# Kernel tuning notes

Hardware: AMD Instinct MI355X
Metric: run time of the kernel (lower is better)

## Reference

```python
import jax, jax.numpy as jnp
import numpy as np

HEADS = 4
DIM_HEAD = 32


def _ln(x, g, b):
    m = x.mean(-1, keepdims=True)
    v = ((x - m) ** 2).mean(-1, keepdims=True)
    return (x - m) * jax.lax.rsqrt(v + 1e-5) * g + b


def setup_inputs() -> dict:
    key = jax.random.key(0)
    ks = jax.random.split(key, 9)
    b, n, X, Y, W1, W2, d = 4, 6, 10, 10, 10, 10, 128
    x, y, w1, w2 = 10, 10, 4, 4
    inner = HEADS * DIM_HEAD  # 128 == d
    init = 0.02
    return {
        "q": jax.random.normal(ks[0], (b, n, X, Y, W1, W2, d), jnp.float32),
        "k": jax.random.normal(ks[1], (b, n, x, y, w1, w2, d), jnp.float32),
        "v": jax.random.normal(ks[2], (b, n, x, y, w1, w2, d), jnp.float32),
        "skip": jax.random.normal(ks[3], (b, X, Y, W1, W2, d), jnp.float32),
        "head_gate": jax.random.uniform(ks[4], (HEADS,), jnp.float32, 0.5, 1.5),
        "ln_q_g": jnp.ones((d,), jnp.float32), "ln_q_b": jnp.zeros((d,), jnp.float32),
        "ln_k_g": jnp.ones((d,), jnp.float32), "ln_k_b": jnp.zeros((d,), jnp.float32),
        "ln_v_g": jnp.ones((d,), jnp.float32), "ln_v_b": jnp.zeros((d,), jnp.float32),
        "wq": jax.random.normal(ks[5], (d, inner), jnp.float32) * init,
        "bq": jnp.zeros((inner,), jnp.float32),
        "wk": jax.random.normal(ks[6], (d, inner), jnp.float32) * init,
        "bk": jnp.zeros((inner,), jnp.float32),
        "wv": jax.random.normal(ks[7], (d, inner), jnp.float32) * init,
        "bv": jnp.zeros((inner,), jnp.float32),
        "wp": jax.random.normal(ks[8], (inner, d), jnp.float32) * init,
        "bp": jnp.zeros((d,), jnp.float32),
    }


def reference(q, k, v, skip, head_gate,
              ln_q_g, ln_q_b, ln_k_g, ln_k_b, ln_v_g, ln_v_b,
              wq, bq, wk, bk, wv, bv, wp, bp):
    b, n, X, Y, W1, W2, d = q.shape
    _, _, x, y, w1, w2, _ = k.shape
    L = X * Y                      # number of windows (== x*y, asserted in torch)
    Qn = n * W1 * W2               # query tokens per window (views folded in)
    Kn = n * w1 * w2               # kv tokens per window
    # 'b n x y w1 w2 d -> b (x y) (n w1 w2) d'
    qf = q.transpose(0, 2, 3, 1, 4, 5, 6).reshape(b, L, Qn, d)
    kf = k.transpose(0, 2, 3, 1, 4, 5, 6).reshape(b, L, Kn, d)
    vf = v.transpose(0, 2, 3, 1, 4, 5, 6).reshape(b, L, Kn, d)
    # pre-norm + linear qkv projections
    qh = (_ln(qf, ln_q_g, ln_q_b) @ wq + bq).reshape(b, L, Qn, HEADS, DIM_HEAD)
    kh = (_ln(kf, ln_k_g, ln_k_b) @ wk + bk).reshape(b, L, Kn, HEADS, DIM_HEAD)
    vh = (_ln(vf, ln_v_g, ln_v_b) @ wv + bv).reshape(b, L, Kn, HEADS, DIM_HEAD)
    scale = DIM_HEAD ** -0.5
    # windowed attention scores: (b, m, L, Q, K)
    dot = jnp.einsum('blqmd,blkmd->bmlqk', qh * scale, kh)
    dot = dot * head_gate[None, :, None, None, None]  # multiplicative head gate pre-softmax
    att = jax.nn.softmax(dot, axis=-1)
    a = jnp.einsum('bmlqk,blkmd->blqmd', att, vh).reshape(b, L, Qn, HEADS * DIM_HEAD)
    # 'b (x y) (n w1 w2) c -> b n x y w1 w2 c'
    out = a.reshape(b, X, Y, n, W1, W2, HEADS * DIM_HEAD).transpose(0, 3, 1, 2, 4, 5, 6)
    z = out @ wp + bp
    z = z.mean(axis=1)             # mean-pool over views
    return z + skip
```

## Files before the change

kernel.cpp:

```cpp
#include <hip/hip_runtime.h>
#include <hip/hip_bf16.h>

#define DEV __device__ __forceinline__

typedef __attribute__((ext_vector_type(8))) short short8;
typedef __attribute__((ext_vector_type(8))) unsigned short ushort8;
typedef __attribute__((ext_vector_type(4))) float f32x4;
typedef __attribute__((ext_vector_type(2))) unsigned int uint2v;

DEV unsigned short f2bf(float f) {
    unsigned u = __float_as_uint(f);
    unsigned r = u + 0x7fffu + ((u >> 16) & 1u);
    return (unsigned short)(r >> 16);
}
DEV unsigned cvt_pk_bf16(float lo, float hi) {
    unsigned r;
    asm("v_cvt_pk_bf16_f32 %0, %1, %2" : "=v"(r) : "v"(lo), "v"(hi));
    return r;
}
#define GLDS16(gp, lp)                                                              \
    __builtin_amdgcn_global_load_lds(                                               \
        (const __attribute__((address_space(1))) void*)(gp),                        \
        (__attribute__((address_space(3))) void*)(lp), 16, 0, 0)


__global__ __launch_bounds__(128) void prep_kernel(
    const float* __restrict__ wq, const float* __restrict__ wk,
    const float* __restrict__ wv, const float* __restrict__ wp,
    const float* __restrict__ ln_q_g, const float* __restrict__ ln_q_b,
    const float* __restrict__ ln_k_g, const float* __restrict__ ln_k_b,
    const float* __restrict__ ln_v_g, const float* __restrict__ ln_v_b,
    const float* __restrict__ bq, const float* __restrict__ bk,
    const float* __restrict__ bv, const float* __restrict__ bp,
    const float* __restrict__ head_gate,
    unsigned short* __restrict__ Wt, float* __restrict__ b2)
{
    const int set = blockIdx.x / 9, sub = blockIdx.x % 9;
    const float* W    = set == 0 ? wq : set == 1 ? wk : set == 2 ? wv : wp;
    const float* g    = set == 0 ? ln_q_g : set == 1 ? ln_k_g : ln_v_g;
    const float* e    = set == 0 ? ln_q_b : set == 1 ? ln_k_b : ln_v_b;
    const float* bias = set == 0 ? bq : set == 1 ? bk : set == 2 ? bv : bp;
    const int mode = set == 0 ? 2 : (set == 3 ? 0 : 1);
    const float scale = 0.17677669529663687f;

    if (sub == 0) {
        const int col = threadIdx.x;
        float sg = (mode == 2) ? scale * head_gate[col >> 5] : 1.f;
        float esum = 0.f;
        if (mode >= 1) {
#pragma unroll 8
            for (int k = 0; k < 128; ++k) esum += e[k] * W[k * 128 + col];
        }
        b2[set * 128 + col] = (bias[col] + esum) * sg;
    } else {
        const int k = threadIdx.x;
        const float gk = (mode >= 1) ? g[k] : 1.f;
        const int kk = k >> 5, h = (k >> 3) & 3, j = k & 7;
#pragma unroll
        for (int c = 0; c < 16; ++c) {
            int col = (sub - 1) * 16 + c;
            int nt = col >> 4, q15 = col & 15;
            float sg = (mode == 2) ? scale * head_gate[col >> 5] : 1.f;
            long idx = set * 16384 + (((nt * 4 + kk) * 64 + q15 * 4 + h) << 3) + j;
            Wt[idx] = f2bf(W[k * 128 + col] * gk * sg);
        }
    }
}

__global__ __launch_bounds__(256) void qkv_proj_mfma(
    const float* __restrict__ qsrc, const float* __restrict__ ksrc, const float* __restrict__ vsrc,
    const unsigned short* __restrict__ WtAll, const float* __restrict__ b2All,
    unsigned short* __restrict__ qh, unsigned short* __restrict__ kh, unsigned short* __restrict__ vh)
{
    __shared__ unsigned short WtL[16384];

    const int bid = blockIdx.x;
    const int tid = threadIdx.x;
    const int w = tid >> 6, lane = tid & 63;
    const int q15 = lane & 15, h = lane >> 4;

    const float* src; unsigned short* dst; int set, isQ, grp;
    if (bid < 4200)      { src = qsrc; dst = qh; set = 0; isQ = 1; grp = bid * 4 + w; }
    else if (bid < 4800) { src = ksrc; dst = kh; set = 1; isQ = 0; grp = (bid - 4200) * 4 + w; }
    else                 { src = vsrc; dst = vh; set = 2; isQ = 0; grp = (bid - 4800) * 4 + w; }
    const unsigned short* WtF = WtAll + set * 16384;
    const float* b2 = b2All + set * 128;

#pragma unroll
    for (int i = 0; i < 8; ++i)
        GLDS16(WtF + i * 2048 + tid * 8, &WtL[i * 2048 + w * 512]);

    int so;
    if (isQ) {
        int bl = grp / 42, rem = grp % 42;
        int nn = rem / 7, t = rem % 7;
        int rc = t * 16 + q15; if (rc > 99) rc = 99;
        int b = bl / 100, l = bl % 100;
        int Xi = l / 10, Yi = l % 10;
        int wA = rc / 10, wB = rc % 10;
        so = ((((b * 6 + nn) * 10 + Xi) * 10 + Yi) * 10 + wA) * 10 + wB;
    } else {
        int bl = grp / 6, nn = grp % 6;
        int b = bl / 100, l = bl % 100;
        int Xi = l / 10, Yi = l % 10;
        int wA = q15 >> 2, wB = q15 & 3;
        so = ((((b * 6 + nn) * 10 + Xi) * 10 + Yi) * 4 + wA) * 4 + wB;
    }

    float x[4][8];
    {
        const float* row = src + (long)so * 128 + h * 8;
#pragma unroll
        for (int kk = 0; kk < 4; ++kk) {
            f32x4 a = *(const f32x4*)(row + kk * 32);
            f32x4 b = *(const f32x4*)(row + kk * 32 + 4);
            x[kk][0] = a[0]; x[kk][1] = a[1]; x[kk][2] = a[2]; x[kk][3] = a[3];
            x[kk][4] = b[0]; x[kk][5] = b[1]; x[kk][6] = b[2]; x[kk][7] = b[3];
        }
    }

    float s = 0.f, s2 = 0.f;
#pragma unroll
    for (int kk = 0; kk < 4; ++kk)
#pragma unroll
        for (int j = 0; j < 8; ++j) { s += x[kk][j]; s2 += x[kk][j] * x[kk][j]; }
    s  += __shfl_xor(s, 16);  s  += __shfl_xor(s, 32);
    s2 += __shfl_xor(s2, 16); s2 += __shfl_xor(s2, 32);
    const float mean = s * (1.f / 128.f);
    const float var  = s2 * (1.f / 128.f) - mean * mean;
    const float rs  = rsqrtf(var + 1e-5f);
    const float mrs = -mean * rs;

    short8 xf[4];
#pragma unroll
    for (int kk = 0; kk < 4; ++kk) {
        union { unsigned u[4]; short8 s8; } cv;
#pragma unroll
        for (int d = 0; d < 4; ++d)
            cv.u[d] = cvt_pk_bf16(fmaf(x[kk][2 * d], rs, mrs), fmaf(x[kk][2 * d + 1], rs, mrs));
        xf[kk] = cv.s8;
    }

    f32x4 acc[8];
#pragma unroll
    for (int nt = 0; nt < 8; ++nt)
        acc[nt] = *(const f32x4*)(b2 + nt * 16 + h * 4);

    __syncthreads();

#pragma unroll
    for (int kk = 0; kk < 4; ++kk)
#pragma unroll
        for (int nt = 0; nt < 8; ++nt) {
            short8 wf = *(const short8*)&WtL[(((nt * 4 + kk) * 64) + lane) * 8];
            acc[nt] = __builtin_amdgcn_mfma_f32_16x16x32_bf16(wf, xf[kk], acc[nt], 0, 0, 0);
        }

    unsigned short* og = dst + (long)grp * 1024;
#pragma unroll
    for (int nt = 0; nt < 8; ++nt) {
        uint2v pk;
        pk.x = cvt_pk_bf16(acc[nt][0], acc[nt][1]);
        pk.y = cvt_pk_bf16(acc[nt][2], acc[nt][3]);
        *(uint2v*)(og + (nt * 64 + q15 * 4 + h) * 4) = pk;
    }
}

__global__ __launch_bounds__(256, 3) void attn_mfma_kernel(
    const unsigned short* __restrict__ qh, const unsigned short* __restrict__ kh,
    const unsigned short* __restrict__ vh, unsigned short* __restrict__ am)
{
    __shared__ unsigned short Vt[32 * 104];
    __shared__ unsigned short Pt[4][2][16 * 104];

    const int tid = threadIdx.x;
    const int half = blockIdx.x & 1;
    const int m  = (blockIdx.x >> 1) & 3;
    const int bl = blockIdx.x >> 3;
    const int w = tid >> 6, lane = tid & 63;
    const int q15 = lane & 15, h = lane >> 4;
    const int t = half * 4 + w;

    const int coff = (((2 * m + (h >> 1)) * 64) + q15 * 4 + 2 * (h & 1)) * 4;

    short8 kf[6];
#pragma unroll
    for (int ntk = 0; ntk < 6; ++ntk)
        kf[ntk] = *(const short8*)(kh + (long)(bl * 6 + ntk) * 1024 + coff);

    {
        const int d = tid & 31, kt0 = tid >> 5;
        const int f = m * 32 + d;
        const int ntv = f >> 4, hp = (f >> 2) & 3, rg = f & 3;
#pragma unroll
        for (int j = 0; j < 12; ++j) {
            int kt = kt0 + 8 * j;
            Vt[d * 104 + kt] =
                vh[(long)(bl * 6 + (kt >> 4)) * 1024 + ((ntv * 64 + (kt & 15) * 4 + hp) << 2) + rg];
        }
    }
    __syncthreads();

    short8 vf[2][3];
#pragma unroll
    for (int dt = 0; dt < 2; ++dt)
#pragma unroll
        for (int ks = 0; ks < 3; ++ks)
            vf[dt][ks] = *(const short8*)(Vt + (dt * 16 + q15) * 104 + ks * 32 + h * 8);

    if (t >= 7) return;

    const long qgBase = (long)(bl * 6) * 7 * 1024;

    f32x4 o0 = {0.f, 0.f, 0.f, 0.f}, o1 = {0.f, 0.f, 0.f, 0.f};

#pragma unroll
    for (int nn = 0; nn < 6; ++nn) {
        unsigned short* ptw = &Pt[w][nn & 1][0];

        short8 qf = *(const short8*)(qh + qgBase + (long)(nn * 7 + t) * 1024 + coff);

        f32x4 sc[6];
#pragma unroll
        for (int nt = 0; nt < 6; ++nt)
            sc[nt] = __builtin_amdgcn_mfma_f32_16x16x32_bf16(kf[nt], qf, (f32x4){0.f, 0.f, 0.f, 0.f}, 0, 0, 0);

        float p[24];
#pragma unroll
        for (int nt = 0; nt < 6; ++nt)
#pragma unroll
            for (int rg = 0; rg < 4; ++rg)
                p[nt * 4 + rg] = __expf(sc[nt][rg]);

#pragma unroll
        for (int nt = 0; nt < 6; ++nt) {
            uint2v pk;
            pk.x = cvt_pk_bf16(p[nt * 4 + 0], p[nt * 4 + 1]);
            pk.y = cvt_pk_bf16(p[nt * 4 + 2], p[nt * 4 + 3]);
            *(uint2v*)(ptw + q15 * 104 + nt * 16 + h * 4) = pk;
        }

        float s01 = (p[0] + p[1]) + (p[2] + p[3]);
        float s23 = (p[4] + p[5]) + (p[6] + p[7]);
        float s45 = (p[8] + p[9]) + (p[10] + p[11]);
        float s67 = (p[12] + p[13]) + (p[14] + p[15]);
        float s89 = (p[16] + p[17]) + (p[18] + p[19]);
        float sab = (p[20] + p[21]) + (p[22] + p[23]);
        float sum = ((s01 + s23) + (s45 + s67)) + (s89 + sab);
        sum += __shfl_xor(sum, 16);
        sum += __shfl_xor(sum, 32);
        const float inv = __builtin_amdgcn_rcpf(6.f * sum);

        f32x4 t0 = {0.f, 0.f, 0.f, 0.f}, t1 = {0.f, 0.f, 0.f, 0.f};
#pragma unroll
        for (int ks = 0; ks < 3; ++ks) {
            short8 pf = *(const short8*)(ptw + q15 * 104 + ks * 32 + h * 8);
            t0 = __builtin_amdgcn_mfma_f32_16x16x32_bf16(vf[0][ks], pf, t0, 0, 0, 0);
            t1 = __builtin_amdgcn_mfma_f32_16x16x32_bf16(vf[1][ks], pf, t1, 0, 0, 0);
        }

#pragma unroll
        for (int rg = 0; rg < 4; ++rg) {
            o0[rg] += t0[rg] * inv;
            o1[rg] += t1[rg] * inv;
        }
    }

    {
        unsigned short* og = am + (long)(bl * 7 + t) * 1024;
        uint2v a0, a1;
        a0.x = cvt_pk_bf16(o0[0], o0[1]);
        a0.y = cvt_pk_bf16(o0[2], o0[3]);
        a1.x = cvt_pk_bf16(o1[0], o1[1]);
        a1.y = cvt_pk_bf16(o1[2], o1[3]);
        *(uint2v*)(og + ((2 * m) * 64 + q15 * 4 + h) * 4) = a0;
        *(uint2v*)(og + ((2 * m + 1) * 64 + q15 * 4 + h) * 4) = a1;
    }
}

__global__ __launch_bounds__(256) void out_proj_mfma(
    const unsigned short* __restrict__ am, const unsigned short* __restrict__ WtF,
    const float* __restrict__ b2, const float* __restrict__ skip, float* __restrict__ out)
{
    __shared__ unsigned short WtL[16384];

    const int tid = threadIdx.x;
    const int w = tid >> 6, lane = tid & 63;
    const int q15 = lane & 15, h = lane >> 4;
    const int gp = blockIdx.x * 4 + w;
    const int bl = gp / 7, t = gp % 7;
    const int r = t * 16 + q15;
    const long tok = (long)bl * 100 + r;

#pragma unroll
    for (int i = 0; i < 8; ++i)
        GLDS16(WtF + i * 2048 + tid * 8, &WtL[i * 2048 + w * 512]);

    short8 xf[4];
#pragma unroll
    for (int kk = 0; kk < 4; ++kk)
        xf[kk] = *(const short8*)(am + (long)gp * 1024 +
                                  (((2 * kk + (h >> 1)) * 64 + q15 * 4 + 2 * (h & 1)) << 2));

    f32x4 acc[8];
#pragma unroll
    for (int nt = 0; nt < 8; ++nt)
        acc[nt] = *(const f32x4*)(b2 + nt * 16 + h * 4);

    __syncthreads();

#pragma unroll
    for (int kk = 0; kk < 4; ++kk)
#pragma unroll
        for (int nt = 0; nt < 8; ++nt) {
            short8 wf = *(const short8*)&WtL[(((nt * 4 + kk) * 64) + lane) * 8];
            acc[nt] = __builtin_amdgcn_mfma_f32_16x16x32_bf16(wf, xf[kk], acc[nt], 0, 0, 0);
        }

    if (r < 100) {
        const float* srow = skip + tok * 128 + h * 4;
        float* orow = out + tok * 128 + h * 4;
#pragma unroll
        for (int nt = 0; nt < 8; ++nt) {
            f32x4 sk = *(const f32x4*)(srow + nt * 16);
            f32x4 o;
#pragma unroll
            for (int rg = 0; rg < 4; ++rg) o[rg] = acc[nt][rg] + sk[rg];
            *(f32x4*)(orow + nt * 16) = o;
        }
    }
}

extern "C" void kernel_launch(void* const* d_in, const int* in_sizes, int n_in,
                              void* d_out, int out_size, void* d_ws, size_t ws_size,
                              hipStream_t stream) {
    const float* q        = (const float*)d_in[0];
    const float* k        = (const float*)d_in[1];
    const float* v        = (const float*)d_in[2];
    const float* skip     = (const float*)d_in[3];
    const float* head_gate= (const float*)d_in[4];
    const float* ln_q_g   = (const float*)d_in[5];
    const float* ln_q_b   = (const float*)d_in[6];
    const float* ln_k_g   = (const float*)d_in[7];
    const float* ln_k_b   = (const float*)d_in[8];
    const float* ln_v_g   = (const float*)d_in[9];
    const float* ln_v_b   = (const float*)d_in[10];
    const float* wq       = (const float*)d_in[11];
    const float* bq       = (const float*)d_in[12];
    const float* wk       = (const float*)d_in[13];
    const float* bk       = (const float*)d_in[14];
    const float* wv       = (const float*)d_in[15];
    const float* bv       = (const float*)d_in[16];
    const float* wp       = (const float*)d_in[17];
    const float* bp       = (const float*)d_in[18];
    float* out = (float*)d_out;

    char* ws = (char*)d_ws;
    unsigned short* qh = (unsigned short*)(ws);
    unsigned short* kh = (unsigned short*)(ws + 34406400);
    unsigned short* vh = (unsigned short*)(ws + 39321600);
    unsigned short* am = (unsigned short*)(ws + 44236800);
    unsigned short* Wt = (unsigned short*)(ws + 49971200);
    float* b2          = (float*)(ws + 50102272);

    prep_kernel<<<36, 128, 0, stream>>>(wq, wk, wv, wp,
                                        ln_q_g, ln_q_b, ln_k_g, ln_k_b, ln_v_g, ln_v_b,
                                        bq, bk, bv, bp, head_gate, Wt, b2);
    qkv_proj_mfma<<<5400, 256, 0, stream>>>(q, k, v, Wt, b2, qh, kh, vh);
    attn_mfma_kernel<<<3200, 256, 0, stream>>>(qh, kh, vh, am);
    out_proj_mfma<<<700, 256, 0, stream>>>(am, Wt + 3 * 16384, b2 + 3 * 128, skip, out);
}
```

Before: 88.40 us.

## Make QKV projection blocks persistent over 8 groups with double-buffered input loads

```diff
diff --git a/kernel.cpp b/kernel.cpp
--- a/kernel.cpp
+++ b/kernel.cpp
@@ -79,10 +79,10 @@
     const int w = tid >> 6, lane = tid & 63;
     const int q15 = lane & 15, h = lane >> 4;
 
-    const float* src; unsigned short* dst; int set, isQ, grp;
-    if (bid < 4200)      { src = qsrc; dst = qh; set = 0; isQ = 1; grp = bid * 4 + w; }
-    else if (bid < 4800) { src = ksrc; dst = kh; set = 1; isQ = 0; grp = (bid - 4200) * 4 + w; }
-    else                 { src = vsrc; dst = vh; set = 2; isQ = 0; grp = (bid - 4800) * 4 + w; }
+    const float* src; unsigned short* dst; int set, isQ, gbase;
+    if (bid < 525)      { src = qsrc; dst = qh; set = 0; isQ = 1; gbase = bid * 32; }
+    else if (bid < 600) { src = ksrc; dst = kh; set = 1; isQ = 0; gbase = (bid - 525) * 32; }
+    else                { src = vsrc; dst = vh; set = 2; isQ = 0; gbase = (bid - 600) * 32; }
     const unsigned short* WtF = WtAll + set * 16384;
     const float* b2 = b2All + set * 128;
 
@@ -90,79 +90,101 @@
     for (int i = 0; i < 8; ++i)
         GLDS16(WtF + i * 2048 + tid * 8, &WtL[i * 2048 + w * 512]);
 
-    int so;
-    if (isQ) {
-        int bl = grp / 42, rem = grp % 42;
-        int nn = rem / 7, t = rem % 7;
-        int rc = t * 16 + q15; if (rc > 99) rc = 99;
-        int b = bl / 100, l = bl % 100;
-        int Xi = l / 10, Yi = l % 10;
-        int wA = rc / 10, wB = rc % 10;
-        so = ((((b * 6 + nn) * 10 + Xi) * 10 + Yi) * 10 + wA) * 10 + wB;
-    } else {
-        int bl = grp / 6, nn = grp % 6;
-        int b = bl / 100, l = bl % 100;
-        int Xi = l / 10, Yi = l % 10;
-        int wA = q15 >> 2, wB = q15 & 3;
-        so = ((((b * 6 + nn) * 10 + Xi) * 10 + Yi) * 4 + wA) * 4 + wB;
-    }
-
-    float x[4][8];
+    auto srcRow = [&](int grp) -> const float* {
+        int so;
+        if (isQ) {
+            int bl = grp / 42, rem = grp % 42;
+            int nn = rem / 7, t = rem % 7;
+            int rc = t * 16 + q15; if (rc > 99) rc = 99;
+            int b = bl / 100, l = bl % 100;
+            int Xi = l / 10, Yi = l % 10;
+            int wA = rc / 10, wB = rc % 10;
+            so = ((((b * 6 + nn) * 10 + Xi) * 10 + Yi) * 10 + wA) * 10 + wB;
+        } else {
+            int bl = grp / 6, nn = grp % 6;
+            int b = bl / 100, l = bl % 100;
+            int Xi = l / 10, Yi = l % 10;
+            int wA = q15 >> 2, wB = q15 & 3;
+            so = ((((b * 6 + nn) * 10 + Xi) * 10 + Yi) * 4 + wA) * 4 + wB;
+        }
+        return src + (long)so * 128 + h * 8;
+    };
+
+    f32x4 xs[2][8];
     {
-        const float* row = src + (long)so * 128 + h * 8;
+        const float* row = srcRow(gbase + w);
 #pragma unroll
         for (int kk = 0; kk < 4; ++kk) {
-            f32x4 a = *(const f32x4*)(row + kk * 32);
-            f32x4 b = *(const f32x4*)(row + kk * 32 + 4);
-            x[kk][0] = a[0]; x[kk][1] = a[1]; x[kk][2] = a[2]; x[kk][3] = a[3];
-            x[kk][4] = b[0]; x[kk][5] = b[1]; x[kk][6] = b[2]; x[kk][7] = b[3];
-        }
-    }
-
-    float s = 0.f, s2 = 0.f;
-#pragma unroll
-    for (int kk = 0; kk < 4; ++kk)
-#pragma unroll
-        for (int j = 0; j < 8; ++j) { s += x[kk][j]; s2 += x[kk][j] * x[kk][j]; }
-    s  += __shfl_xor(s, 16);  s  += __shfl_xor(s, 32);
-    s2 += __shfl_xor(s2, 16); s2 += __shfl_xor(s2, 32);
-    const float mean = s * (1.f / 128.f);
-    const float var  = s2 * (1.f / 128.f) - mean * mean;
-    const float rs  = rsqrtf(var + 1e-5f);
-    const float mrs = -mean * rs;
-
-    short8 xf[4];
-#pragma unroll
-    for (int kk = 0; kk < 4; ++kk) {
-        union { unsigned u[4]; short8 s8; } cv;
-#pragma unroll
-        for (int d = 0; d < 4; ++d)
-            cv.u[d] = cvt_pk_bf16(fmaf(x[kk][2 * d], rs, mrs), fmaf(x[kk][2 * d + 1], rs, mrs));
-        xf[kk] = cv.s8;
-    }
-
-    f32x4 acc[8];
-#pragma unroll
-    for (int nt = 0; nt < 8; ++nt)
-        acc[nt] = *(const f32x4*)(b2 + nt * 16 + h * 4);
+            xs[0][2 * kk]     = *(const f32x4*)(row + kk * 32);
+            xs[0][2 * kk + 1] = *(const f32x4*)(row + kk * 32 + 4);
+        }
+    }
 
     __syncthreads();
 
 #pragma unroll
-    for (int kk = 0; kk < 4; ++kk)
+    for (int i = 0; i < 8; ++i) {
+        const int cur = i & 1, nxt = cur ^ 1;
+        const int grp = gbase + i * 4 + w;
+
+        if (i < 7) {
+            const float* row = srcRow(gbase + (i + 1) * 4 + w);
+#pragma unroll
+            for (int kk = 0; kk < 4; ++kk) {
+                xs[nxt][2 * kk]     = *(const f32x4*)(row + kk * 32);
+                xs[nxt][2 * kk + 1] = *(const f32x4*)(row + kk * 32 + 4);
+            }
+        }
+
+        float s = 0.f, s2 = 0.f;
+#pragma unroll
+        for (int j = 0; j < 8; ++j)
+#pragma unroll
+            for (int c = 0; c < 4; ++c) {
+                float v = xs[cur][j][c];
+                s += v; s2 += v * v;
+            }
+        s  += __shfl_xor(s, 16);  s  += __shfl_xor(s, 32);
+        s2 += __shfl_xor(s2, 16); s2 += __shfl_xor(s2, 32);
+        const float mean = s * (1.f / 128.f);
+        const float var  = s2 * (1.f / 128.f) - mean * mean;
+        const float rs  = rsqrtf(var + 1e-5f);
+        const float mrs = -mean * rs;
+
+        short8 xf[4];
+#pragma unroll
+        for (int kk = 0; kk < 4; ++kk) {
+            union { unsigned u[4]; short8 s8; } cv;
+#pragma unroll
+            for (int d = 0; d < 2; ++d) {
+                f32x4 a = xs[cur][2 * kk + d];
+                cv.u[2 * d]     = cvt_pk_bf16(fmaf(a[0], rs, mrs), fmaf(a[1], rs, mrs));
+                cv.u[2 * d + 1] = cvt_pk_bf16(fmaf(a[2], rs, mrs), fmaf(a[3], rs, mrs));
+            }
+            xf[kk] = cv.s8;
+        }
+
+        f32x4 acc[8];
+#pragma unroll
+        for (int nt = 0; nt < 8; ++nt)
+            acc[nt] = *(const f32x4*)(b2 + nt * 16 + h * 4);
+
+#pragma unroll
+        for (int kk = 0; kk < 4; ++kk)
+#pragma unroll
+            for (int nt = 0; nt < 8; ++nt) {
+                short8 wf = *(const short8*)&WtL[(((nt * 4 + kk) * 64) + lane) * 8];
+                acc[nt] = __builtin_amdgcn_mfma_f32_16x16x32_bf16(wf, xf[kk], acc[nt], 0, 0, 0);
+            }
+
+        unsigned short* og = dst + (long)grp * 1024;
 #pragma unroll
         for (int nt = 0; nt < 8; ++nt) {
-            short8 wf = *(const short8*)&WtL[(((nt * 4 + kk) * 64) + lane) * 8];
-            acc[nt] = __builtin_amdgcn_mfma_f32_16x16x32_bf16(wf, xf[kk], acc[nt], 0, 0, 0);
-        }
-
-    unsigned short* og = dst + (long)grp * 1024;
-#pragma unroll
-    for (int nt = 0; nt < 8; ++nt) {
-        uint2v pk;
-        pk.x = cvt_pk_bf16(acc[nt][0], acc[nt][1]);
-        pk.y = cvt_pk_bf16(acc[nt][2], acc[nt][3]);
-        *(uint2v*)(og + (nt * 64 + q15 * 4 + h) * 4) = pk;
+            uint2v pk;
+            pk.x = cvt_pk_bf16(acc[nt][0], acc[nt][1]);
+            pk.y = cvt_pk_bf16(acc[nt][2], acc[nt][3]);
+            *(uint2v*)(og + (nt * 64 + q15 * 4 + h) * 4) = pk;
+        }
     }
 }
 
@@ -366,7 +388,7 @@
     prep_kernel<<<36, 128, 0, stream>>>(wq, wk, wv, wp,
                                         ln_q_g, ln_q_b, ln_k_g, ln_k_b, ln_v_g, ln_v_b,
                                         bq, bk, bv, bp, head_gate, Wt, b2);
-    qkv_proj_mfma<<<5400, 256, 0, stream>>>(q, k, v, Wt, b2, qh, kh, vh);
+    qkv_proj_mfma<<<675, 256, 0, stream>>>(q, k, v, Wt, b2, qh, kh, vh);
     attn_mfma_kernel<<<3200, 256, 0, stream>>>(qh, kh, vh, am);
     out_proj_mfma<<<700, 256, 0, stream>>>(am, Wt + 3 * 16384, b2 + 3 * 128, skip, out);
 }
```

After: 90.08 us. No clear change (+1.9%).
